# Performance work log

Hardware: AMD Instinct MI355X
Metric: run time of the kernel (lower is better)

## Reference

```python
import jax, jax.numpy as jnp
import numpy as np

EPS = 1e-6     # vnn EPS
BN_EPS = 1e-5  # torch BatchNorm eps


def _vn_batchnorm(x, gamma, beta):
    # x: (B, C, 3, ...). BatchNorm on vector norms (training-mode batch stats).
    norm = jnp.linalg.norm(x, axis=2) + EPS                # (B, C, ...)
    axes = (0,) + tuple(range(2, norm.ndim))
    mean = norm.mean(axis=axes, keepdims=True)
    var = norm.var(axis=axes, keepdims=True)               # biased var, as torch training BN
    shape = (1, -1) + (1,) * (norm.ndim - 2)
    norm_bn = (norm - mean) / jnp.sqrt(var + BN_EPS) * gamma.reshape(shape) + beta.reshape(shape)
    return x / jnp.expand_dims(norm, 2) * jnp.expand_dims(norm_bn, 2)


def _vn_linear_leaky(x, Wf, Wd, gamma, beta):
    # VNLinearLeakyReLU with negative_slope = 0.0
    p = jnp.einsum('oc,bc...->bo...', Wf, x)
    p = _vn_batchnorm(p, gamma, beta)
    d = jnp.einsum('oc,bc...->bo...', Wd, x)
    dot = jnp.sum(p * d, axis=2, keepdims=True)
    dsq = jnp.sum(d * d, axis=2, keepdims=True)
    mask = (dot >= 0).astype(x.dtype)
    return mask * p + (1.0 - mask) * (p - (dot / (dsq + EPS)) * d)


def _graph_feature_cross(x, k):
    # x: (B, 3, N) -> (B, 3, 3, N, k)  channels = [nbr - x, x, x cross nbr]
    xt = jnp.swapaxes(x, 1, 2)                             # (B, N, 3)
    inner = -2.0 * jnp.einsum('bnc,bmc->bnm', xt, xt)      # (B, N, N)
    xx = jnp.sum(x * x, axis=1)                            # (B, N)
    pd = -xx[:, :, None] - inner - xx[:, None, :]          # negative squared distance
    idx = jax.lax.top_k(pd, k)[1]                          # (B, N, k)
    nbr = jax.vmap(lambda pts, i: pts[i])(xt, idx)         # (B, N, k, 3)
    nbr = nbr[:, :, :, None, :]                            # (B, N, k, 1, 3)
    ctr = jnp.broadcast_to(xt[:, :, None, None, :], nbr.shape)
    cross = jnp.cross(nbr, ctr)
    feat = jnp.concatenate([nbr - ctr, ctr, cross], axis=3)  # (B, N, k, 3, 3)
    return jnp.transpose(feat, (0, 3, 4, 1, 2))            # (B, 3, 3, N, k)


def _forward(point_cloud, Wf0, Wd0, g0, b0, Wf1, Wd1, g1, b1, gbn1, bbn1, Wf2, Wd2, g2, b2):
    x = jnp.swapaxes(point_cloud, 1, 2)                    # (B, 3, N)
    num_points = x.shape[1]                                # = 3, faithful to source
    k = min(5, num_points - 1)                             # = 2
    feat = _graph_feature_cross(x, k)                      # (B, 3, 3, N, k)
    out = _vn_linear_leaky(feat, Wf0, Wd0, g0, b0)         # (B, 21, 3, N, k)
    out = out.mean(axis=-1)                                # mean_pool over k -> (B, 21, 3, N)
    out = _vn_linear_leaky(out, Wf1, Wd1, g1, b1)
    out = _vn_batchnorm(out, gbn1, bbn1)
    out = _vn_linear_leaky(out, Wf2, Wd2, g2, b2)          # (B, 4, 3, N)
    # dropout: eval-mode identity
    return out.mean(axis=-1)[:, :3]                        # (B, 3, 3)


def setup_inputs() -> dict:
    key = jax.random.key(0)
    ks = jax.random.split(key, 8)
    B, N = 16, 4096
    C = 21  # 64 // 3
    Co = 4  # 12 // 3
    f32 = jnp.float32
    s3 = 1.0 / np.sqrt(3.0)
    sC = 1.0 / np.sqrt(C)
    return {
        'point_cloud': jax.random.normal(ks[0], (B, N, 3), f32),
        'Wf0': jax.random.normal(ks[1], (C, 3), f32) * s3,
        'Wd0': jax.random.normal(ks[2], (C, 3), f32) * s3,
        'g0': jnp.ones((C,), f32), 'b0': jnp.zeros((C,), f32),
        'Wf1': jax.random.normal(ks[3], (C, C), f32) * sC,
        'Wd1': jax.random.normal(ks[4], (C, C), f32) * sC,
        'g1': jnp.ones((C,), f32), 'b1': jnp.zeros((C,), f32),
        'gbn1': jnp.ones((C,), f32), 'bbn1': jnp.zeros((C,), f32),
        'Wf2': jax.random.normal(ks[5], (Co, C), f32) * sC,
        'Wd2': jax.random.normal(ks[6], (Co, C), f32) * sC,
        'g2': jnp.ones((Co,), f32), 'b2': jnp.zeros((Co,), f32),
    }


def reference(point_cloud, Wf0, Wd0, g0, b0, Wf1, Wd1, g1, b1, gbn1, bbn1, Wf2, Wd2, g2, b2):
    return _forward(point_cloud, Wf0, Wd0, g0, b0, Wf1, Wd1, g1, b1, gbn1, bbn1, Wf2, Wd2, g2, b2)
```

## Files before the change

kernel.cpp:

```cpp
#include <hip/hip_runtime.h>
#include <math.h>

#define B 16
#define N 4096
#define NPTS (B * N)
#define NBK 2048
#define NBT 1024
#define EPSF 1e-6f
#define S8(i) ((i) * 8)

__device__ __forceinline__ float waveReduceSum(float v) {
#pragma unroll
    for (int m = 32; m > 0; m >>= 1) v += __shfl_xor(v, m, 64);
    return v;
}

__device__ __forceinline__ void leaky3(float px, float py, float pz,
                                       float dx, float dy, float dz, float s,
                                       float& ox, float& oy, float& oz) {
    float dotr = px * dx + py * dy + pz * dz;
    float dsq = dx * dx + dy * dy + dz * dz;
    float dot = s * dotr;
    float coef = (dot >= 0.f) ? 0.f : (dot / (dsq + EPSF));
    ox = s * px - coef * dx;
    oy = s * py - coef * dy;
    oz = s * pz - coef * dz;
}

__device__ __forceinline__ void mk_muisd(const double* st, int cnt, double M,
                                         float* smu, float* sisd) {
    const int i = threadIdx.x;
    if (i < cnt) {
        double m = st[S8(i)] / M;
        double v = st[S8(cnt + i)] / M - m * m;
        smu[i] = (float)m;
        sisd[i] = (float)(1.0 / sqrt(v + 1e-5));
    }
}

struct Feat {
    float cx, cy, cz, e0x, e0y, e0z, e2x, e2y, e2z;
};

__device__ __forceinline__ Feat make_feat(const float* __restrict__ pc,
                                          const int* __restrict__ nbr, int pid) {
    const int b = pid >> 12, n = pid & (N - 1);
    const float* base = pc + (size_t)b * (3 * N);
    Feat f;
    f.cx = base[3 * n];
    f.cy = base[3 * n + 1];
    f.cz = base[3 * n + 2];
    const int jn = nbr[pid];
    float nx = base[3 * jn], ny = base[3 * jn + 1], nz = base[3 * jn + 2];
    f.e0x = nx - f.cx;
    f.e0y = ny - f.cy;
    f.e0z = nz - f.cz;
    f.e2x = ny * f.cz - nz * f.cy;
    f.e2y = nz * f.cx - nx * f.cz;
    f.e2z = nx * f.cy - ny * f.cx;
    return f;
}

#define QW 8
__global__ __launch_bounds__(256) void k_knn(const float* __restrict__ pc,
                                             const float* __restrict__ Wf0,
                                             int* __restrict__ nbrbest,
                                             double* __restrict__ st0) {
    __shared__ float sx[N], sy[N], sz[N];
    __shared__ float ws0[63], sred[168];
    const int b = blockIdx.x >> 7;
    const int qblk = (blockIdx.x & 127) * 32;
    const float* base = pc + (size_t)b * (N * 3);
    for (int j = threadIdx.x; j < N; j += 256) {
        sx[j] = base[3 * j + 0];
        sy[j] = base[3 * j + 1];
        sz[j] = base[3 * j + 2];
    }
    if (threadIdx.x < 63) ws0[threadIdx.x] = Wf0[threadIdx.x];
    __syncthreads();
    const int wid = threadIdx.x >> 6, lane = threadIdx.x & 63;
    const int q0 = qblk + wid * QW;
    float qx[QW], qy[QW], qz[QW], bv[QW];
    int bi[QW], bq[QW];
#pragma unroll
    for (int q = 0; q < QW; ++q) {
        qx[q] = sx[q0 + q];
        qy[q] = sy[q0 + q];
        qz[q] = sz[q0 + q];
        bv[q] = -3.0e38f;
        bi[q] = 0;
    }
#pragma unroll 4
    for (int ch = 0; ch < N / 64; ++ch) {
        const int j = ch * 64 + lane;
        const float xd = sx[j], yd = sy[j], zd = sz[j];
        const float nr2h = -0.5f * (xd * xd + yd * yd + zd * zd);
#pragma unroll
        for (int q = 0; q < QW; ++q) {
            float pd = fmaf(qx[q], xd, fmaf(qy[q], yd, fmaf(qz[q], zd, nr2h)));
            bool upd = (pd > bv[q]) && (j != q0 + q);
            bv[q] = upd ? pd : bv[q];
            bi[q] = upd ? j : bi[q];
        }
    }
#pragma unroll
    for (int q = 0; q < QW; ++q) {
        float a0v = bv[q], a1v = -3.0e38f;
        int a0i = bi[q], a1i = 0x7fffffff;
#pragma unroll
        for (int m = 1; m < 64; m <<= 1) {
            float b0v = __shfl_xor(a0v, m, 64), b1v = __shfl_xor(a1v, m, 64);
            int b0i = __shfl_xor(a0i, m, 64), b1i = __shfl_xor(a1i, m, 64);
            bool bf = (b0v > a0v) || (b0v == a0v && b0i < a0i);
            float c0v = bf ? a0v : b0v;
            int c0i = bf ? a0i : b0i;
            float c1v = bf ? b1v : a1v;
            int c1i = bf ? b1i : a1i;
            a0v = bf ? b0v : a0v;
            a0i = bf ? b0i : a0i;
            bool cf = (c0v > c1v) || (c0v == c1v && c0i < c1i);
            a1v = cf ? c0v : c1v;
            a1i = cf ? c0i : c1i;
        }
        const int i0 = a0i, i1 = a1i;
        double dxa = (double)qx[q] - (double)sx[i0];
        double dya = (double)qy[q] - (double)sy[i0];
        double dza = (double)qz[q] - (double)sz[i0];
        double d0 = dxa * dxa + dya * dya + dza * dza;
        double dxb = (double)qx[q] - (double)sx[i1];
        double dyb = (double)qy[q] - (double)sy[i1];
        double dzb = (double)qz[q] - (double)sz[i1];
        double d1 = dxb * dxb + dyb * dyb + dzb * dzb;
        bool take1 = (d1 < d0) || (d1 == d0 && i1 < i0);
        int best = take1 ? i1 : i0;
        bq[q] = best;
        if (lane == 0) nbrbest[(size_t)b * N + q0 + q] = best;
    }
    if (lane < 21) {
        float s1 = 0.f, s2 = 0.f;
        const float w0 = ws0[3 * lane], w1 = ws0[3 * lane + 1], w2 = ws0[3 * lane + 2];
#pragma unroll
        for (int q = 0; q < QW; ++q) {
            const int sq = q0 + q, jn = bq[q];
            const float cx = sx[sq], cy = sy[sq], cz = sz[sq];
            const float nx = sx[jn], ny = sy[jn], nz = sz[jn];
            const float e0x = nx - cx, e0y = ny - cy, e0z = nz - cz;
            const float e2x = ny * cz - nz * cy;
            const float e2y = nz * cx - nx * cz;
            const float e2z = nx * cy - ny * cx;
            float pSx = w1 * cx, pSy = w1 * cy, pSz = w1 * cz;
            float nS = sqrtf(pSx * pSx + pSy * pSy + pSz * pSz) + EPSF;
            float px = w0 * e0x + w1 * cx + w2 * e2x;
            float py = w0 * e0y + w1 * cy + w2 * e2y;
            float pz = w0 * e0z + w1 * cz + w2 * e2z;
            float nN = sqrtf(px * px + py * py + pz * pz) + EPSF;
            s1 += nS + nN;
            s2 += nS * nS + nN * nN;
        }
        sred[wid * 42 + lane] = s1;
        sred[wid * 42 + 21 + lane] = s2;
    }
    __syncthreads();
    if (threadIdx.x < 42) {
        float p = sred[threadIdx.x] + sred[42 + threadIdx.x] +
                  sred[84 + threadIdx.x] + sred[126 + threadIdx.x];
        atomicAdd(&st0[S8(threadIdx.x)], (double)p);
    }
}

__global__ __launch_bounds__(256) void k_l0st1(
    const float* __restrict__ pc, const int* __restrict__ nbr,
    const float* __restrict__ Wf0, const float* __restrict__ Wd0,
    const float* __restrict__ g0, const float* __restrict__ b0,
    const float* __restrict__ Wf1, const double* __restrict__ st0,
    float* __restrict__ xbuf, double* __restrict__ st1) {
    __shared__ float wf0[63], wd0[63], wf1[441], gg[21], bbs[21], mu[21], isd[21];
    __shared__ float xs[63 * 64];
    if (threadIdx.x < 63) {
        wf0[threadIdx.x] = Wf0[threadIdx.x];
        wd0[threadIdx.x] = Wd0[threadIdx.x];
    }
    for (int i = threadIdx.x; i < 441; i += 256) wf1[i] = Wf1[i];
    if (threadIdx.x < 21) {
        gg[threadIdx.x] = g0[threadIdx.x];
        bbs[threadIdx.x] = b0[threadIdx.x];
    }
    mk_muisd(st0, 21, (double)NPTS * 2.0, mu, isd);
    __syncthreads();
    const int lane = threadIdx.x & 63, grp = threadIdx.x >> 6;
    const int pid = blockIdx.x * 64 + lane;
    Feat f = make_feat(pc, nbr, pid);
    const int cbase = grp * 6;
#pragma unroll
    for (int k = 0; k < 6; ++k) {
        const int c = cbase + k;
        if (c >= 21) break;
        float w0 = wf0[3 * c], w1 = wf0[3 * c + 1], w2 = wf0[3 * c + 2];
        float u0 = wd0[3 * c], u1 = wd0[3 * c + 1], u2 = wd0[3 * c + 2];
        float pSx = w1 * f.cx, pSy = w1 * f.cy, pSz = w1 * f.cz;
        float nS = sqrtf(pSx * pSx + pSy * pSy + pSz * pSz) + EPSF;
        float sS = ((nS - mu[c]) * isd[c] * gg[c] + bbs[c]) / nS;
        float oSx, oSy, oSz;
        leaky3(pSx, pSy, pSz, u1 * f.cx, u1 * f.cy, u1 * f.cz, sS, oSx, oSy, oSz);
        float px = w0 * f.e0x + w1 * f.cx + w2 * f.e2x;
        float py = w0 * f.e0y + w1 * f.cy + w2 * f.e2y;
        float pz = w0 * f.e0z + w1 * f.cz + w2 * f.e2z;
        float dx = u0 * f.e0x + u1 * f.cx + u2 * f.e2x;
        float dy = u0 * f.e0y + u1 * f.cy + u2 * f.e2y;
        float dz = u0 * f.e0z + u1 * f.cz + u2 * f.e2z;
        float nN = sqrtf(px * px + py * py + pz * pz) + EPSF;
        float sN = ((nN - mu[c]) * isd[c] * gg[c] + bbs[c]) / nN;
        float oNx, oNy, oNz;
        leaky3(px, py, pz, dx, dy, dz, sN, oNx, oNy, oNz);
        float x0 = 0.5f * (oSx + oNx), x1 = 0.5f * (oSy + oNy), x2 = 0.5f * (oSz + oNz);
        xs[(3 * c + 0) * 64 + lane] = x0;
        xs[(3 * c + 1) * 64 + lane] = x1;
        xs[(3 * c + 2) * 64 + lane] = x2;
        xbuf[(size_t)(3 * c + 0) * NPTS + pid] = x0;
        xbuf[(size_t)(3 * c + 1) * NPTS + pid] = x1;
        xbuf[(size_t)(3 * c + 2) * NPTS + pid] = x2;
    }
    __syncthreads();
    float xl[63];
#pragma unroll
    for (int ff = 0; ff < 63; ++ff) xl[ff] = xs[ff * 64 + lane];
#pragma unroll
    for (int k = 0; k < 6; ++k) {
        const int c = cbase + k;
        if (c >= 21) break;
        float p0 = 0.f, p1 = 0.f, p2 = 0.f;
#pragma unroll
        for (int j = 0; j < 21; ++j) {
            float w = wf1[c * 21 + j];
            p0 = fmaf(w, xl[3 * j + 0], p0);
            p1 = fmaf(w, xl[3 * j + 1], p1);
            p2 = fmaf(w, xl[3 * j + 2], p2);
        }
        float nn = sqrtf(p0 * p0 + p1 * p1 + p2 * p2) + EPSF;
        float r1 = waveReduceSum(nn);
        float r2 = waveReduceSum(nn * nn);
        if (lane == 0) {
            atomicAdd(&st1[S8(c)], (double)r1);
            atomicAdd(&st1[S8(21 + c)], (double)r2);
        }
    }
}

__global__ __launch_bounds__(256) void k_l1stB(
    float* __restrict__ xbuf, const float* __restrict__ Wf1,
    const float* __restrict__ Wd1, const float* __restrict__ g1,
    const float* __restrict__ b1, const double* __restrict__ st1,
    double* __restrict__ stB) {
    __shared__ float wf1[441], wd1[441], gg[21], bbs[21], mu[21], isd[21];
    for (int i = threadIdx.x; i < 441; i += 256) {
        wf1[i] = Wf1[i];
        wd1[i] = Wd1[i];
    }
    if (threadIdx.x < 21) {
        gg[threadIdx.x] = g1[threadIdx.x];
        bbs[threadIdx.x] = b1[threadIdx.x];
    }
    mk_muisd(st1, 21, (double)NPTS, mu, isd);
    __syncthreads();
    const int lane = threadIdx.x & 63, grp = threadIdx.x >> 6;
    const int pid = blockIdx.x * 64 + lane;
    float xl[63];
#pragma unroll
    for (int ff = 0; ff < 63; ++ff) xl[ff] = xbuf[(size_t)ff * NPTS + pid];
    __syncthreads();
    const int cbase = grp * 6;
#pragma unroll
    for (int k = 0; k < 6; ++k) {
        const int c = cbase + k;
        if (c >= 21) break;
        float p0 = 0.f, p1 = 0.f, p2 = 0.f, d0 = 0.f, d1 = 0.f, d2 = 0.f;
#pragma unroll
        for (int j = 0; j < 21; ++j) {
            float w = wf1[c * 21 + j], u = wd1[c * 21 + j];
            p0 = fmaf(w, xl[3 * j + 0], p0);
            p1 = fmaf(w, xl[3 * j + 1], p1);
            p2 = fmaf(w, xl[3 * j + 2], p2);
            d0 = fmaf(u, xl[3 * j + 0], d0);
            d1 = fmaf(u, xl[3 * j + 1], d1);
            d2 = fmaf(u, xl[3 * j + 2], d2);
        }
        float nn = sqrtf(p0 * p0 + p1 * p1 + p2 * p2) + EPSF;
        float s = ((nn - mu[c]) * isd[c] * gg[c] + bbs[c]) / nn;
        float ox, oy, oz;
        leaky3(p0, p1, p2, d0, d1, d2, s, ox, oy, oz);
        xbuf[(size_t)(3 * c + 0) * NPTS + pid] = ox;
        xbuf[(size_t)(3 * c + 1) * NPTS + pid] = oy;
        xbuf[(size_t)(3 * c + 2) * NPTS + pid] = oz;
        float on = sqrtf(ox * ox + oy * oy + oz * oz) + EPSF;
        float r1 = waveReduceSum(on);
        float r2 = waveReduceSum(on * on);
        if (lane == 0) {
            atomicAdd(&stB[S8(c)], (double)r1);
            atomicAdd(&stB[S8(21 + c)], (double)r2);
        }
    }
}

__global__ __launch_bounds__(256) void k_bn1st2(
    float* __restrict__ xbuf, const float* __restrict__ gbn,
    const float* __restrict__ bbn, const float* __restrict__ Wf2,
    const double* __restrict__ stB, double* __restrict__ st2) {
    __shared__ float wf2[63], gg[21], bbs[21], mu[21], isd[21];
    __shared__ float zs[63 * 64];
    if (threadIdx.x < 63) wf2[threadIdx.x] = Wf2[threadIdx.x];
    if (threadIdx.x < 21) {
        gg[threadIdx.x] = gbn[threadIdx.x];
        bbs[threadIdx.x] = bbn[threadIdx.x];
    }
    mk_muisd(stB, 21, (double)NPTS, mu, isd);
    __syncthreads();
    const int lane = threadIdx.x & 63, grp = threadIdx.x >> 6;
    const int pid = blockIdx.x * 64 + lane;
    const int cbase = grp * 6;
#pragma unroll
    for (int k = 0; k < 6; ++k) {
        const int c = cbase + k;
        if (c >= 21) break;
        float y0 = xbuf[(size_t)(3 * c + 0) * NPTS + pid];
        float y1 = xbuf[(size_t)(3 * c + 1) * NPTS + pid];
        float y2 = xbuf[(size_t)(3 * c + 2) * NPTS + pid];
        float nn = sqrtf(y0 * y0 + y1 * y1 + y2 * y2) + EPSF;
        float sc = ((nn - mu[c]) * isd[c] * gg[c] + bbs[c]) / nn;
        y0 *= sc; y1 *= sc; y2 *= sc;
        zs[(3 * c + 0) * 64 + lane] = y0;
        zs[(3 * c + 1) * 64 + lane] = y1;
        zs[(3 * c + 2) * 64 + lane] = y2;
        xbuf[(size_t)(3 * c + 0) * NPTS + pid] = y0;
        xbuf[(size_t)(3 * c + 1) * NPTS + pid] = y1;
        xbuf[(size_t)(3 * c + 2) * NPTS + pid] = y2;
    }
    __syncthreads();
    if (grp < 3) {
        float p0 = 0.f, p1 = 0.f, p2 = 0.f;
#pragma unroll
        for (int j = 0; j < 21; ++j) {
            float w = wf2[grp * 21 + j];
            p0 = fmaf(w, zs[(3 * j + 0) * 64 + lane], p0);
            p1 = fmaf(w, zs[(3 * j + 1) * 64 + lane], p1);
            p2 = fmaf(w, zs[(3 * j + 2) * 64 + lane], p2);
        }
        float nn = sqrtf(p0 * p0 + p1 * p1 + p2 * p2) + EPSF;
        float r1 = waveReduceSum(nn);
        float r2 = waveReduceSum(nn * nn);
        if (lane == 0) {
            atomicAdd(&st2[S8(grp)], (double)r1);
            atomicAdd(&st2[S8(3 + grp)], (double)r2);
        }
    }
}

__global__ __launch_bounds__(256) void k_acc(
    const float* __restrict__ xbuf, const float* __restrict__ Wf2,
    const float* __restrict__ Wd2, const float* __restrict__ g2,
    const float* __restrict__ b2, const double* __restrict__ st2,
    double* __restrict__ acc) {
    __shared__ float wf2[63], wd2[63], gg[3], bbs[3], mu[3], isd[3];
    if (threadIdx.x < 63) {
        wf2[threadIdx.x] = Wf2[threadIdx.x];
        wd2[threadIdx.x] = Wd2[threadIdx.x];
    }
    if (threadIdx.x < 3) {
        gg[threadIdx.x] = g2[threadIdx.x];
        bbs[threadIdx.x] = b2[threadIdx.x];
    }
    mk_muisd(st2, 3, (double)NPTS, mu, isd);
    __syncthreads();
    const int lane = threadIdx.x & 63, grp = threadIdx.x >> 6;
    if (grp >= 3) return;
    const int pid = blockIdx.x * 64 + lane;
    const int b = pid >> 12;
    float p0 = 0.f, p1 = 0.f, p2 = 0.f, d0 = 0.f, d1 = 0.f, d2 = 0.f;
#pragma unroll
    for (int j = 0; j < 21; ++j) {
        float x0 = xbuf[(size_t)(3 * j + 0) * NPTS + pid];
        float x1 = xbuf[(size_t)(3 * j + 1) * NPTS + pid];
        float x2 = xbuf[(size_t)(3 * j + 2) * NPTS + pid];
        float w = wf2[grp * 21 + j], u = wd2[grp * 21 + j];
        p0 = fmaf(w, x0, p0);
        p1 = fmaf(w, x1, p1);
        p2 = fmaf(w, x2, p2);
        d0 = fmaf(u, x0, d0);
        d1 = fmaf(u, x1, d1);
        d2 = fmaf(u, x2, d2);
    }
    float nn = sqrtf(p0 * p0 + p1 * p1 + p2 * p2) + EPSF;
    float s = ((nn - mu[grp]) * isd[grp] * gg[grp] + bbs[grp]) / nn;
    float ox, oy, oz;
    leaky3(p0, p1, p2, d0, d1, d2, s, ox, oy, oz);
    float rx = waveReduceSum(ox);
    float ry = waveReduceSum(oy);
    float rz = waveReduceSum(oz);
    if (lane == 0) {
        atomicAdd(&acc[S8(b * 9 + grp * 3 + 0)], (double)rx);
        atomicAdd(&acc[S8(b * 9 + grp * 3 + 1)], (double)ry);
        atomicAdd(&acc[S8(b * 9 + grp * 3 + 2)], (double)rz);
    }
}

__global__ void k_fin(const double* __restrict__ acc, float* __restrict__ out) {
    if (threadIdx.x < B * 9)
        out[threadIdx.x] = (float)(acc[S8(threadIdx.x)] * (1.0 / (double)N));
}

extern "C" void kernel_launch(void* const* d_in, const int* in_sizes, int n_in,
                              void* d_out, int out_size, void* d_ws, size_t ws_size,
                              hipStream_t stream) {
    const float* pc = (const float*)d_in[0];
    const float* Wf0 = (const float*)d_in[1];
    const float* Wd0 = (const float*)d_in[2];
    const float* g0 = (const float*)d_in[3];
    const float* b0 = (const float*)d_in[4];
    const float* Wf1 = (const float*)d_in[5];
    const float* Wd1 = (const float*)d_in[6];
    const float* g1 = (const float*)d_in[7];
    const float* b1 = (const float*)d_in[8];
    const float* gbn1 = (const float*)d_in[9];
    const float* bbn1 = (const float*)d_in[10];
    const float* Wf2 = (const float*)d_in[11];
    const float* Wd2 = (const float*)d_in[12];
    const float* g2 = (const float*)d_in[13];
    const float* b2 = (const float*)d_in[14];
    float* out = (float*)d_out;

    char* ws = (char*)d_ws;
    double* gws = (double*)ws;
    double* st0 = gws;
    double* st1 = gws + 336;
    double* stB = gws + 672;
    double* st2 = gws + 1008;
    double* acc = gws + 1056;
    int* nbrbest = (int*)(ws + 32768);
    float* xbuf = (float*)(ws + 32768 + 262144);

    hipMemsetAsync(d_ws, 0, 17664, stream);

    k_knn<<<NBK, 256, 0, stream>>>(pc, Wf0, nbrbest, st0);
    k_l0st1<<<NBT, 256, 0, stream>>>(pc, nbrbest, Wf0, Wd0, g0, b0, Wf1, st0,
                                     xbuf, st1);
    k_l1stB<<<NBT, 256, 0, stream>>>(xbuf, Wf1, Wd1, g1, b1, st1, stB);
    k_bn1st2<<<NBT, 256, 0, stream>>>(xbuf, gbn1, bbn1, Wf2, stB, st2);
    k_acc<<<NBT, 256, 0, stream>>>(xbuf, Wf2, Wd2, g2, b2, st2, acc);
    k_fin<<<1, 256, 0, stream>>>(acc, out);
}
```

Measured before the change: 273.7 us.

## Shard BN stat atomics per batch and recompute BN1 in final kernel

BatchNorm statistic accumulators are split into per-batch slots, each padded to a separate cache line, and consumers sum the 16 slots when computing mean and inverse std. This spreads atomic contention that previously hit a single address per channel. The bn1 kernel also stops writing normalized values back to xbuf; the final kernel instead recomputes the BN1 scaling from stB on the fly. That trades a 63-channel global write for extra per-point sqrt and divide work, and makes the workspace memset larger.

```diff
diff --git a/kernel.cpp b/kernel.cpp
--- a/kernel.cpp
+++ b/kernel.cpp
@@ -27,12 +27,18 @@
     oz = s * pz - coef * dz;
 }
 
-__device__ __forceinline__ void mk_muisd(const double* st, int cnt, double M,
-                                         float* smu, float* sisd) {
+__device__ __forceinline__ void mk_muisd_b(const double* st, int cnt, double M,
+                                           float* smu, float* sisd) {
     const int i = threadIdx.x;
     if (i < cnt) {
-        double m = st[S8(i)] / M;
-        double v = st[S8(cnt + i)] / M - m * m;
+        double s1 = 0.0, s2 = 0.0;
+#pragma unroll
+        for (int b = 0; b < B; ++b) {
+            s1 += st[S8(b * 2 * cnt + i)];
+            s2 += st[S8(b * 2 * cnt + cnt + i)];
+        }
+        double m = s1 / M;
+        double v = s2 / M - m * m;
         smu[i] = (float)m;
         sisd[i] = (float)(1.0 / sqrt(v + 1e-5));
     }
@@ -164,7 +170,7 @@
     if (threadIdx.x < 42) {
         float p = sred[threadIdx.x] + sred[42 + threadIdx.x] +
                   sred[84 + threadIdx.x] + sred[126 + threadIdx.x];
-        atomicAdd(&st0[S8(threadIdx.x)], (double)p);
+        atomicAdd(&st0[S8(b * 42 + threadIdx.x)], (double)p);
     }
 }
 
@@ -185,10 +191,11 @@
         gg[threadIdx.x] = g0[threadIdx.x];
         bbs[threadIdx.x] = b0[threadIdx.x];
     }
-    mk_muisd(st0, 21, (double)NPTS * 2.0, mu, isd);
+    mk_muisd_b(st0, 21, (double)NPTS * 2.0, mu, isd);
     __syncthreads();
     const int lane = threadIdx.x & 63, grp = threadIdx.x >> 6;
     const int pid = blockIdx.x * 64 + lane;
+    const int bb = blockIdx.x >> 6;
     Feat f = make_feat(pc, nbr, pid);
     const int cbase = grp * 6;
 #pragma unroll
@@ -240,8 +247,8 @@
         float r1 = waveReduceSum(nn);
         float r2 = waveReduceSum(nn * nn);
         if (lane == 0) {
-            atomicAdd(&st1[S8(c)], (double)r1);
-            atomicAdd(&st1[S8(21 + c)], (double)r2);
+            atomicAdd(&st1[S8(bb * 42 + c)], (double)r1);
+            atomicAdd(&st1[S8(bb * 42 + 21 + c)], (double)r2);
         }
     }
 }
@@ -260,10 +267,11 @@
         gg[threadIdx.x] = g1[threadIdx.x];
         bbs[threadIdx.x] = b1[threadIdx.x];
     }
-    mk_muisd(st1, 21, (double)NPTS, mu, isd);
+    mk_muisd_b(st1, 21, (double)NPTS, mu, isd);
     __syncthreads();
     const int lane = threadIdx.x & 63, grp = threadIdx.x >> 6;
     const int pid = blockIdx.x * 64 + lane;
+    const int bb = blockIdx.x >> 6;
     float xl[63];
 #pragma unroll
     for (int ff = 0; ff < 63; ++ff) xl[ff] = xbuf[(size_t)ff * NPTS + pid];
@@ -295,14 +303,14 @@
         float r1 = waveReduceSum(on);
         float r2 = waveReduceSum(on * on);
         if (lane == 0) {
-            atomicAdd(&stB[S8(c)], (double)r1);
-            atomicAdd(&stB[S8(21 + c)], (double)r2);
+            atomicAdd(&stB[S8(bb * 42 + c)], (double)r1);
+            atomicAdd(&stB[S8(bb * 42 + 21 + c)], (double)r2);
         }
     }
 }
 
 __global__ __launch_bounds__(256) void k_bn1st2(
-    float* __restrict__ xbuf, const float* __restrict__ gbn,
+    const float* __restrict__ xbuf, const float* __restrict__ gbn,
     const float* __restrict__ bbn, const float* __restrict__ Wf2,
     const double* __restrict__ stB, double* __restrict__ st2) {
     __shared__ float wf2[63], gg[21], bbs[21], mu[21], isd[21];
@@ -312,10 +320,11 @@
         gg[threadIdx.x] = gbn[threadIdx.x];
         bbs[threadIdx.x] = bbn[threadIdx.x];
     }
-    mk_muisd(stB, 21, (double)NPTS, mu, isd);
+    mk_muisd_b(stB, 21, (double)NPTS, mu, isd);
     __syncthreads();
     const int lane = threadIdx.x & 63, grp = threadIdx.x >> 6;
     const int pid = blockIdx.x * 64 + lane;
+    const int bb = blockIdx.x >> 6;
     const int cbase = grp * 6;
 #pragma unroll
     for (int k = 0; k < 6; ++k) {
@@ -326,13 +335,9 @@
         float y2 = xbuf[(size_t)(3 * c + 2) * NPTS + pid];
         float nn = sqrtf(y0 * y0 + y1 * y1 + y2 * y2) + EPSF;
         float sc = ((nn - mu[c]) * isd[c] * gg[c] + bbs[c]) / nn;
-        y0 *= sc; y1 *= sc; y2 *= sc;
-        zs[(3 * c + 0) * 64 + lane] = y0;
-        zs[(3 * c + 1) * 64 + lane] = y1;
-        zs[(3 * c + 2) * 64 + lane] = y2;
-        xbuf[(size_t)(3 * c + 0) * NPTS + pid] = y0;
-        xbuf[(size_t)(3 * c + 1) * NPTS + pid] = y1;
-        xbuf[(size_t)(3 * c + 2) * NPTS + pid] = y2;
+        zs[(3 * c + 0) * 64 + lane] = sc * y0;
+        zs[(3 * c + 1) * 64 + lane] = sc * y1;
+        zs[(3 * c + 2) * 64 + lane] = sc * y2;
     }
     __syncthreads();
     if (grp < 3) {
@@ -348,57 +353,67 @@
         float r1 = waveReduceSum(nn);
         float r2 = waveReduceSum(nn * nn);
         if (lane == 0) {
-            atomicAdd(&st2[S8(grp)], (double)r1);
-            atomicAdd(&st2[S8(3 + grp)], (double)r2);
+            atomicAdd(&st2[S8(bb * 6 + grp)], (double)r1);
+            atomicAdd(&st2[S8(bb * 6 + 3 + grp)], (double)r2);
         }
     }
 }
 
 __global__ __launch_bounds__(256) void k_acc(
-    const float* __restrict__ xbuf, const float* __restrict__ Wf2,
+    const float* __restrict__ xbuf, const float* __restrict__ gbn,
+    const float* __restrict__ bbn, const float* __restrict__ Wf2,
     const float* __restrict__ Wd2, const float* __restrict__ g2,
-    const float* __restrict__ b2, const double* __restrict__ st2,
-    double* __restrict__ acc) {
-    __shared__ float wf2[63], wd2[63], gg[3], bbs[3], mu[3], isd[3];
+    const float* __restrict__ b2, const double* __restrict__ stB,
+    const double* __restrict__ st2, double* __restrict__ acc) {
+    __shared__ float wf2[63], wd2[63], gg[3], bbs[3];
+    __shared__ float muB[21], isdB[21], gB[21], bB[21], mu2[3], isd2[3];
     if (threadIdx.x < 63) {
         wf2[threadIdx.x] = Wf2[threadIdx.x];
         wd2[threadIdx.x] = Wd2[threadIdx.x];
     }
+    if (threadIdx.x < 21) {
+        gB[threadIdx.x] = gbn[threadIdx.x];
+        bB[threadIdx.x] = bbn[threadIdx.x];
+    }
     if (threadIdx.x < 3) {
         gg[threadIdx.x] = g2[threadIdx.x];
         bbs[threadIdx.x] = b2[threadIdx.x];
     }
-    mk_muisd(st2, 3, (double)NPTS, mu, isd);
+    mk_muisd_b(stB, 21, (double)NPTS, muB, isdB);
+    mk_muisd_b(st2, 3, (double)NPTS, mu2, isd2);
     __syncthreads();
     const int lane = threadIdx.x & 63, grp = threadIdx.x >> 6;
     if (grp >= 3) return;
     const int pid = blockIdx.x * 64 + lane;
-    const int b = pid >> 12;
+    const int bb = pid >> 12;
     float p0 = 0.f, p1 = 0.f, p2 = 0.f, d0 = 0.f, d1 = 0.f, d2 = 0.f;
 #pragma unroll
     for (int j = 0; j < 21; ++j) {
-        float x0 = xbuf[(size_t)(3 * j + 0) * NPTS + pid];
-        float x1 = xbuf[(size_t)(3 * j + 1) * NPTS + pid];
-        float x2 = xbuf[(size_t)(3 * j + 2) * NPTS + pid];
+        float y0 = xbuf[(size_t)(3 * j + 0) * NPTS + pid];
+        float y1 = xbuf[(size_t)(3 * j + 1) * NPTS + pid];
+        float y2 = xbuf[(size_t)(3 * j + 2) * NPTS + pid];
+        float nn = sqrtf(y0 * y0 + y1 * y1 + y2 * y2) + EPSF;
+        float sc = ((nn - muB[j]) * isdB[j] * gB[j] + bB[j]) / nn;
+        float z0 = sc * y0, z1 = sc * y1, z2 = sc * y2;
         float w = wf2[grp * 21 + j], u = wd2[grp * 21 + j];
-        p0 = fmaf(w, x0, p0);
-        p1 = fmaf(w, x1, p1);
-        p2 = fmaf(w, x2, p2);
-        d0 = fmaf(u, x0, d0);
-        d1 = fmaf(u, x1, d1);
-        d2 = fmaf(u, x2, d2);
+        p0 = fmaf(w, z0, p0);
+        p1 = fmaf(w, z1, p1);
+        p2 = fmaf(w, z2, p2);
+        d0 = fmaf(u, z0, d0);
+        d1 = fmaf(u, z1, d1);
+        d2 = fmaf(u, z2, d2);
     }
     float nn = sqrtf(p0 * p0 + p1 * p1 + p2 * p2) + EPSF;
-    float s = ((nn - mu[grp]) * isd[grp] * gg[grp] + bbs[grp]) / nn;
+    float s = ((nn - mu2[grp]) * isd2[grp] * gg[grp] + bbs[grp]) / nn;
     float ox, oy, oz;
     leaky3(p0, p1, p2, d0, d1, d2, s, ox, oy, oz);
     float rx = waveReduceSum(ox);
     float ry = waveReduceSum(oy);
     float rz = waveReduceSum(oz);
     if (lane == 0) {
-        atomicAdd(&acc[S8(b * 9 + grp * 3 + 0)], (double)rx);
-        atomicAdd(&acc[S8(b * 9 + grp * 3 + 1)], (double)ry);
-        atomicAdd(&acc[S8(b * 9 + grp * 3 + 2)], (double)rz);
+        atomicAdd(&acc[S8(bb * 9 + grp * 3 + 0)], (double)rx);
+        atomicAdd(&acc[S8(bb * 9 + grp * 3 + 1)], (double)ry);
+        atomicAdd(&acc[S8(bb * 9 + grp * 3 + 2)], (double)rz);
     }
 }
 
@@ -430,20 +445,20 @@
     char* ws = (char*)d_ws;
     double* gws = (double*)ws;
     double* st0 = gws;
-    double* st1 = gws + 336;
-    double* stB = gws + 672;
-    double* st2 = gws + 1008;
-    double* acc = gws + 1056;
-    int* nbrbest = (int*)(ws + 32768);
-    float* xbuf = (float*)(ws + 32768 + 262144);
-
-    hipMemsetAsync(d_ws, 0, 17664, stream);
+    double* st1 = gws + S8(672);
+    double* stB = gws + S8(1344);
+    double* st2 = gws + S8(2016);
+    double* acc = gws + S8(2112);
+    int* nbrbest = (int*)(ws + 262144);
+    float* xbuf = (float*)(ws + 524288);
+
+    hipMemsetAsync(d_ws, 0, 144384, stream);
 
     k_knn<<<NBK, 256, 0, stream>>>(pc, Wf0, nbrbest, st0);
     k_l0st1<<<NBT, 256, 0, stream>>>(pc, nbrbest, Wf0, Wd0, g0, b0, Wf1, st0,
                                      xbuf, st1);
     k_l1stB<<<NBT, 256, 0, stream>>>(xbuf, Wf1, Wd1, g1, b1, st1, stB);
     k_bn1st2<<<NBT, 256, 0, stream>>>(xbuf, gbn1, bbn1, Wf2, stB, st2);
-    k_acc<<<NBT, 256, 0, stream>>>(xbuf, Wf2, Wd2, g2, b2, st2, acc);
+    k_acc<<<NBT, 256, 0, stream>>>(xbuf, gbn1, bbn1, Wf2, Wd2, g2, b2, stB, st2, acc);
     k_fin<<<1, 256, 0, stream>>>(acc, out);
 }
```

Result: faster. 222.7 us (-18.6%).
